# Kernel tuning notes

Measured on AMD Instinct MI355X. Metric: run time of the kernel, lower is better.

## Reference

```python
import jax, jax.numpy as jnp
import numpy as np

N_WIRES = 10
N_BLOCKS = 4
BATCH = 8192
FEAT = 4 * N_WIRES
DIM = 2 ** N_WIRES
BN_EPS = 1e-5

# sign of PauliZ on wire i for each basis state index (wire 0 = most significant bit,
# matching torchquantum's [bsz, 2, 2, ..., 2] state layout)
_k = np.arange(DIM)
_bits = (_k[None, :] >> (N_WIRES - 1 - np.arange(N_WIRES))[:, None]) & 1
SIGNS = jnp.asarray(1.0 - 2.0 * _bits, dtype=jnp.float32)  # [n_wires, 2^n]

H_GATE = jnp.array([[1, 1], [1, -1]], dtype=jnp.complex64) * jnp.complex64(0.70710678)
SX_GATE = jnp.complex64(0.5) * jnp.array([[1 + 1j, 1 - 1j], [1 - 1j, 1 + 1j]], dtype=jnp.complex64)


def rx_mat(theta):
    t = jnp.asarray(theta) * 0.5
    c = jnp.cos(t).astype(jnp.complex64)
    s = (-1j) * jnp.sin(t).astype(jnp.complex64)
    return jnp.stack([jnp.stack([c, s], -1), jnp.stack([s, c], -1)], -2)


def ry_mat(theta):
    t = jnp.asarray(theta) * 0.5
    c = jnp.cos(t).astype(jnp.complex64)
    s = jnp.sin(t).astype(jnp.complex64)
    return jnp.stack([jnp.stack([c, -s], -1), jnp.stack([s, c], -1)], -2)


def rz_mat(theta):
    e = jnp.exp(jnp.complex64(-0.5j) * jnp.asarray(theta).astype(jnp.complex64))
    z = jnp.zeros_like(e)
    return jnp.stack([jnp.stack([e, z], -1), jnp.stack([z, jnp.conj(e)], -1)], -2)


def apply_1q(state, gate, wire):
    # state: [B, 2, 2, ..., 2]; gate: [2,2] (shared) or [B,2,2] (per-sample encoder)
    s = jnp.moveaxis(state, wire + 1, -1)
    if gate.ndim == 3:
        s = jnp.einsum('bij,b...j->b...i', gate, s)
    else:
        s = jnp.einsum('ij,b...j->b...i', gate, s)
    return jnp.moveaxis(s, -1, wire + 1)


def apply_cnot(state, c, t):
    s = jnp.moveaxis(state, (c + 1, t + 1), (-2, -1))  # [..., ctrl, tgt]
    s = jnp.stack([s[..., 0, :], s[..., 1, ::-1]], axis=-2)
    return jnp.moveaxis(s, (-2, -1), (c + 1, t + 1))


def measure_all_z(state):
    probs = (state.real ** 2 + state.imag ** 2).reshape(state.shape[0], -1)  # [B, 2^n]
    return probs @ SIGNS.T  # [B, n_wires]


def encode(state, feats):
    # GeneralEncoder: per wire i apply rx, ry, rz, rx with data angles feats[:, 4i..4i+3]
    for i in range(N_WIRES):
        state = apply_1q(state, rx_mat(feats[:, 4 * i]), i)
        state = apply_1q(state, ry_mat(feats[:, 4 * i + 1]), i)
        state = apply_1q(state, rz_mat(feats[:, 4 * i + 2]), i)
        state = apply_1q(state, rx_mat(feats[:, 4 * i + 3]), i)
    return state


def qnn(feats, rz1, ry1, rz2, rz3):
    B = feats.shape[0]
    state = jnp.zeros((B, DIM), jnp.complex64).at[:, 0].set(1.0)
    state = state.reshape((B,) + (2,) * N_WIRES)
    for k in range(N_BLOCKS):
        for i in range(N_WIRES):
            state = apply_1q(state, rz_mat(rz1[k, i]), i)
        for i in range(N_WIRES):
            state = apply_1q(state, ry_mat(ry1[k, i]), i)
        for i in range(N_WIRES):
            state = apply_1q(state, rz_mat(rz2[k, i]), i)
        for i in range(N_WIRES):  # circular CNOT ring
            state = apply_cnot(state, i, (i + 1) % N_WIRES)
        if k != N_BLOCKS - 1:
            state = encode(state, feats)
    outs = [measure_all_z(state)]
    for i in range(N_WIRES):
        state = apply_1q(state, H_GATE, i)
    outs.append(measure_all_z(state))
    for i in range(N_WIRES):
        state = apply_1q(state, H_GATE, i)
        state = apply_1q(state, SX_GATE, i)
    outs.append(measure_all_z(state))
    for i in range(N_WIRES):  # only the last rz3 layer is applied in the source
        state = apply_1q(state, rz_mat(rz3[-1, i]), i)
    outs.append(measure_all_z(state))
    return jnp.concatenate(outs, axis=-1)  # [B, 4*n_wires]


def setup_inputs() -> dict:
    key = jax.random.key(0)
    ks = jax.random.split(key, 13)
    pi = np.float32(np.pi)
    w_scale = 1.0 / np.sqrt(np.float32(FEAT))
    return {
        'x': jax.random.normal(ks[0], (BATCH, FEAT), jnp.float32),
        'qlin_w': jax.random.normal(ks[1], (FEAT, FEAT), jnp.float32) * w_scale,
        'qlin_b': jax.random.normal(ks[2], (FEAT,), jnp.float32) * w_scale,
        'bn_gamma': jnp.ones((FEAT,), jnp.float32),
        'bn_beta': jnp.zeros((FEAT,), jnp.float32),
        'clin_w': jax.random.normal(ks[3], (FEAT, FEAT), jnp.float32) * w_scale,
        'clin_b': jax.random.normal(ks[4], (FEAT,), jnp.float32) * w_scale,
        'lin_w': jax.random.normal(ks[5], (FEAT, 2 * FEAT), jnp.float32) * w_scale,
        'lin_b': jax.random.normal(ks[6], (FEAT,), jnp.float32) * w_scale,
        'rz1': jax.random.uniform(ks[7], (N_BLOCKS, N_WIRES), jnp.float32, -pi, pi),
        'ry1': jax.random.uniform(ks[8], (N_BLOCKS, N_WIRES), jnp.float32, -pi, pi),
        'rz2': jax.random.uniform(ks[9], (N_BLOCKS, N_WIRES), jnp.float32, -pi, pi),
        'rz3': jax.random.uniform(ks[10], (N_BLOCKS, N_WIRES), jnp.float32, -pi, pi),
    }


def reference(x, qlin_w, qlin_b, bn_gamma, bn_beta, clin_w, clin_b, lin_w, lin_b, rz1, ry1, rz2, rz3):
    # quantum branch: Linear -> BatchNorm1d (training-mode batch stats) -> QNN
    xq = x @ qlin_w.T + qlin_b
    mu = xq.mean(axis=0)
    var = ((xq - mu) ** 2).mean(axis=0)  # biased variance, as torch BN
    xq = (xq - mu) * jax.lax.rsqrt(var + BN_EPS) * bn_gamma + bn_beta
    x1 = qnn(xq, rz1, ry1, rz2, rz3)
    # classical branch
    x2 = jax.nn.relu(x @ clin_w.T + clin_b)
    return jnp.concatenate([x1, x2], axis=-1) @ lin_w.T + lin_b
```

## Files before the change

### kernel.cpp

```cpp
#include <hip/hip_runtime.h>
#include <math.h>


typedef float v2f __attribute__((ext_vector_type(2)));
typedef unsigned uiv2 __attribute__((ext_vector_type(2)));

#define WS_XQ    0
#define WS_X1    327680
#define WS_PS1   327680
#define WS_PS2   368640
#define WS_BNA   655360
#define WS_BNC   655400
#define WS_GATES 655440

__device__ __forceinline__ float bperm1(int addr, float v){
  return __int_as_float(__builtin_amdgcn_ds_bpermute(addr, __float_as_int(v)));
}
__device__ __forceinline__ v2f bperm2(int addr, v2f v){
  v2f r; r.x = bperm1(addr, v.x); r.y = bperm1(addr, v.y); return r;
}
__device__ __forceinline__ v2f vs(float x){ return (v2f){x,x}; }

template<int C>
__device__ __forceinline__ float dppf(float x){
  return __int_as_float(__builtin_amdgcn_update_dpp(0, __float_as_int(x),
                                                    C, 0xf, 0xf, true));
}
#define QP_X1 0xB1
#define QP_X2 0x4E

__device__ __forceinline__ float xor1f(float x, int ){ return dppf<QP_X1>(x); }
__device__ __forceinline__ float xor2f(float x, int ){ return dppf<QP_X2>(x); }

template<int N>
__device__ __forceinline__ float xorshf(float x, int lane){
  float a = dppf<0x110+N>(x);
  float b = dppf<0x100+N>(x);
  return (lane & N) ? a : b;
}
__device__ __forceinline__ float xor4f(float x, int lane){ return xorshf<4>(x,lane); }
__device__ __forceinline__ float xor8f(float x, int lane){ return xorshf<8>(x,lane); }

#if __has_builtin(__builtin_amdgcn_permlane16_swap) && __has_builtin(__builtin_amdgcn_permlane32_swap)
__device__ __forceinline__ float xor16f(float x, int lane){
  uiv2 r = __builtin_amdgcn_permlane16_swap(__float_as_uint(x), __float_as_uint(x),
                                            false, false);
  return __uint_as_float((lane & 16) ? r.x : r.y);
}
__device__ __forceinline__ float xor32f(float x, int lane){
  uiv2 r = __builtin_amdgcn_permlane32_swap(__float_as_uint(x), __float_as_uint(x),
                                            false, false);
  return __uint_as_float((lane & 32) ? r.x : r.y);
}
#else
__device__ __forceinline__ float xor16f(float x, int lane){ return bperm1((lane^16)<<2, x); }
__device__ __forceinline__ float xor32f(float x, int lane){ return bperm1((lane^32)<<2, x); }
#endif

#define DEF_XORV(NAME, F1) \
__device__ __forceinline__ v2f NAME(v2f v, int lane){ \
  v2f r; r.x = F1(v.x,lane); r.y = F1(v.y,lane); return r; }
DEF_XORV(xor1v,  xor1f)
DEF_XORV(xor2v,  xor2f)
DEF_XORV(xor4v,  xor4f)
DEF_XORV(xor8v,  xor8f)
DEF_XORV(xor16v, xor16f)
DEF_XORV(xor32v, xor32f)

__device__ __forceinline__ float dsum(float x){
  x += dppf<0x111>(x);
  x += dppf<0x112>(x);
  x += dppf<0x114>(x);
  x += dppf<0x118>(x);
  x += dppf<0x142>(x);
  x += dppf<0x143>(x);
  return x;
}


#define DEF_GCROSS(NAME, PFN) \
__device__ __forceinline__ void NAME(v2f (&R)[8], v2f (&I)[8], int lane, bool hi, \
                                     const float* g){ \
  const float gar = hi ? g[6] : g[0], gai = hi ? g[7] : g[1]; \
  const float gbr = hi ? g[4] : g[2], gbi = hi ? g[5] : g[3]; \
  const v2f A=vs(gar), B=vs(gai), C=vs(gbr), D=vs(gbi); \
  _Pragma("unroll") \
  for (int p=0;p<8;++p){ \
    v2f PR = PFN(R[p],lane); \
    v2f PI = PFN(I[p],lane); \
    v2f nr = A*R[p] - B*I[p] + C*PR - D*PI; \
    v2f ni = A*I[p] + B*R[p] + C*PI + D*PR; \
    R[p]=nr; I[p]=ni; } \
}
DEF_GCROSS(g_cross_x32, xor32v)
DEF_GCROSS(g_cross_x16, xor16v)
DEF_GCROSS(g_cross_x8,  xor8v)
DEF_GCROSS(g_cross_x4,  xor4v)
DEF_GCROSS(g_cross_x2,  xor2v)
DEF_GCROSS(g_cross_x1,  xor1v)

template<int PM>
__device__ __forceinline__ void g_localp(v2f (&R)[8], v2f (&I)[8], const float* g)
{
  const v2f g00r=vs(g[0]), g00i=vs(g[1]), g01r=vs(g[2]), g01i=vs(g[3]);
  const v2f g10r=vs(g[4]), g10i=vs(g[5]), g11r=vs(g[6]), g11i=vs(g[7]);
#pragma unroll
  for (int p=0;p<8;++p) if (!(p&PM)) {
    const int q = p|PM;
    v2f r0=R[p], i0=I[p], r1=R[q], i1=I[q];
    R[p] = g00r*r0 - g00i*i0 + g01r*r1 - g01i*i1;
    I[p] = g00r*i0 + g00i*r0 + g01r*i1 + g01i*r1;
    R[q] = g10r*r0 - g10i*i0 + g11r*r1 - g11i*i1;
    I[q] = g10r*i0 + g10i*r0 + g11r*i1 + g11i*r1;
  }
}

__device__ __forceinline__ void g_local9(v2f (&R)[8], v2f (&I)[8], const float* g)
{
  const v2f Gr0 = (v2f){g[0], g[4]};
  const v2f Gi0 = (v2f){g[1], g[5]};
  const v2f Gr1 = (v2f){g[2], g[6]};
  const v2f Gi1 = (v2f){g[3], g[7]};
#pragma unroll
  for (int p=0;p<8;++p) {
    v2f Rx = vs(R[p].x), Ix = vs(I[p].x);
    v2f Ry = vs(R[p].y), Iy = vs(I[p].y);
    R[p] = Gr0*Rx - Gi0*Ix + Gr1*Ry - Gi1*Iy;
    I[p] = Gr0*Ix + Gi0*Rx + Gr1*Iy + Gi1*Ry;
  }
}

__device__ __forceinline__ void cnot_ring(v2f (&R)[8], v2f (&I)[8],
                                          int addrg, int lane, bool c5)
{
#pragma unroll
  for (int p=0;p<8;++p) R[p] = bperm2(addrg, R[p]);
#pragma unroll
  for (int p=0;p<8;++p) I[p] = bperm2(addrg, I[p]);
#pragma unroll
  for (int p=0;p<4;++p) {
    v2f a=R[p], b=R[p|4];
    R[p]   = c5 ? b : a;
    R[p|4] = c5 ? a : b;
    v2f ai=I[p], bi=I[p|4];
    I[p]   = c5 ? bi : ai;
    I[p|4] = c5 ? ai : bi;
  }
#pragma unroll
  for (int p=0;p<8;++p) if ((p&4)&&!(p&2)) {
    const int q=p|2;
    v2f t=R[p]; R[p]=R[q]; R[q]=t;
    t=I[p]; I[p]=I[q]; I[q]=t;
  }
#pragma unroll
  for (int p=0;p<8;++p) if ((p&2)&&!(p&1)) {
    const int q=p|1;
    v2f t=R[p]; R[p]=R[q]; R[q]=t;
    t=I[p]; I[p]=I[q]; I[q]=t;
  }
#pragma unroll
  for (int p=1;p<8;p+=2) {
    R[p] = __builtin_shufflevector(R[p],R[p],1,0);
    I[p] = __builtin_shufflevector(I[p],I[p],1,0);
  }
#pragma unroll
  for (int p=0;p<8;++p) {
    R[p].y = xor32f(R[p].y, lane);
    I[p].y = xor32f(I[p].y, lane);
  }
}


__global__ __launch_bounds__(320) void k_xq(const float* __restrict__ x,
                     const float* __restrict__ w, const float* __restrict__ b,
                     float* __restrict__ xq, float* __restrict__ ps1, float* __restrict__ ps2)
{
  __shared__ float wlds[40*41];
  __shared__ float xlds[320];
  __shared__ float accs[320];
  const int t = threadIdx.x;
  const int sl = t/40, f = t - sl*40;
  const int s0 = blockIdx.x*8;
#pragma unroll
  for (int i=0;i<5;++i) {
    int idx = t + i*320;
    int ff = idx/40, kk = idx - ff*40;
    wlds[ff*41+kk] = w[idx];
  }
  xlds[t] = x[s0*40 + t];
  __syncthreads();
  float acc = b[f];
#pragma unroll
  for (int k=0;k<40;++k) acc = fmaf(xlds[sl*40+k], wlds[f*41+k], acc);
  xq[s0*40 + t] = acc;
  accs[t] = acc;
  __syncthreads();
  if (t < 40) {
    float s1=0.f, s2=0.f;
#pragma unroll
    for (int m=0;m<8;++m){ float vv=accs[m*40+t]; s1+=vv; s2=fmaf(vv,vv,s2); }
    ps1[t*1024 + blockIdx.x] = s1;
    ps2[t*1024 + blockIdx.x] = s2;
  }
}

__global__ void k_bn(const float* __restrict__ ps1, const float* __restrict__ ps2,
                     const float* __restrict__ gamma, const float* __restrict__ beta,
                     const float* __restrict__ rz1, const float* __restrict__ ry1,
                     const float* __restrict__ rz2,
                     float* __restrict__ bn_a, float* __restrict__ bn_c,
                     float* __restrict__ gates)
{
  const int f = blockIdx.x, t = threadIdx.x;
  if (f == 40) {
    if (t < 40) {
      float g = rz1[t], a = ry1[t], b = rz2[t];
      float ca, sa, cp, sp, cm, sm;
      sincosf(0.5f*a, &sa, &ca);
      sincosf(0.5f*(b+g), &sp, &cp);
      sincosf(0.5f*(b-g), &sm, &cm);
      float* G = gates + t*8;
      G[0]= ca*cp; G[1]=-ca*sp;
      G[2]=-sa*cm; G[3]= sa*sm;
      G[4]= sa*cm; G[5]= sa*sm;
      G[6]= ca*cp; G[7]= ca*sp;
    }
    return;
  }
  float s1=0.f, s2=0.f;
#pragma unroll
  for (int i=0;i<4;++i){ s1 += ps1[f*1024 + t + i*256]; s2 += ps2[f*1024 + t + i*256]; }
  __shared__ float a1[256], a2[256];
  a1[t]=s1; a2[t]=s2; __syncthreads();
  for (int off=128; off; off>>=1){
    if (t<off){ a1[t]+=a1[t+off]; a2[t]+=a2[t+off]; }
    __syncthreads();
  }
  if (t==0) {
    float mu = a1[0]*(1.f/8192.f);
    float var = a2[0]*(1.f/8192.f) - mu*mu;
    float a = gamma[f]*rsqrtf(var + 1e-5f);
    bn_a[f]=a; bn_c[f]=beta[f]-mu*a;
  }
}

#define GEN10(PTR) \
  g_cross_x32(R,I,lane,h0,(PTR)+0);  g_cross_x16(R,I,lane,h1,(PTR)+8);  \
  g_cross_x8 (R,I,lane,h2,(PTR)+16); g_cross_x4 (R,I,lane,h3,(PTR)+24); \
  g_cross_x2 (R,I,lane,h4,(PTR)+32); g_cross_x1 (R,I,lane,h5,(PTR)+40); \
  g_localp<4>(R,I,(PTR)+48);   g_localp<2>(R,I,(PTR)+56);   \
  g_localp<1>(R,I,(PTR)+64);   g_local9(R,I,(PTR)+72);

__global__ __launch_bounds__(256) void k_qnn(const float* __restrict__ xq,
    const float* __restrict__ bn_a, const float* __restrict__ bn_c,
    const float* __restrict__ gates, float* __restrict__ x1)
{
  const int tix  = threadIdx.x;
  const int lane = tix & 63;
  const int wv   = tix >> 6;
  const int s    = blockIdx.x*4 + wv;

  __shared__ float Ebuf[4][10][8];
  __shared__ float Fbuf[4][3][10][8];

  if (lane < 10) {
    const int i = lane;
    const int f = 4*i;
    float h0 = 0.5f * fmaf(xq[s*40+f+0], bn_a[f+0], bn_c[f+0]);
    float h1 = 0.5f * fmaf(xq[s*40+f+1], bn_a[f+1], bn_c[f+1]);
    float h2 = 0.5f * fmaf(xq[s*40+f+2], bn_a[f+2], bn_c[f+2]);
    float h3 = 0.5f * fmaf(xq[s*40+f+3], bn_a[f+3], bn_c[f+3]);
    float c0,s0,c1,s1,c2,s2,c3,s3;
    sincosf(h0,&s0,&c0); sincosf(h1,&s1,&c1);
    sincosf(h2,&s2,&c2); sincosf(h3,&s3,&c3);
    float A00r=c1*c0, A00i= s1*s0;
    float A01r=-s1*c0, A01i=-c1*s0;
    float A10r= s1*c0, A10i=-c1*s0;
    float A11r= c1*c0, A11i=-s1*s0;
    float B00r = A00r*c2 + A00i*s2, B00i = A00i*c2 - A00r*s2;
    float B01r = A01r*c2 + A01i*s2, B01i = A01i*c2 - A01r*s2;
    float B10r = A10r*c2 - A10i*s2, B10i = A10i*c2 + A10r*s2;
    float B11r = A11r*c2 - A11i*s2, B11i = A11i*c2 + A11r*s2;
    float* e = &Ebuf[wv][i][0];
    e[0] = c3*B00r + s3*B10i;  e[1] = c3*B00i - s3*B10r;
    e[2] = c3*B01r + s3*B11i;  e[3] = c3*B01i - s3*B11r;
    e[4] = c3*B10r + s3*B00i;  e[5] = c3*B10i - s3*B00r;
    e[6] = c3*B11r + s3*B01i;  e[7] = c3*B11i - s3*B01r;
  }

  if (lane < 30) {
    const int k = lane/10, i = lane - k*10;
    const float* U = gates + (k+1)*80 + i*8;
    const float* E = &Ebuf[wv][i][0];
    float u00r=U[0],u00i=U[1],u01r=U[2],u01i=U[3],u10r=U[4],u10i=U[5],u11r=U[6],u11i=U[7];
    float e00r=E[0],e00i=E[1],e01r=E[2],e01i=E[3],e10r=E[4],e10i=E[5],e11r=E[6],e11i=E[7];
    float* F = &Fbuf[wv][k][i][0];
    F[0] = u00r*e00r - u00i*e00i + u01r*e10r - u01i*e10i;
    F[1] = u00r*e00i + u00i*e00r + u01r*e10i + u01i*e10r;
    F[2] = u00r*e01r - u00i*e01i + u01r*e11r - u01i*e11i;
    F[3] = u00r*e01i + u00i*e01r + u01r*e11i + u01i*e11r;
    F[4] = u10r*e00r - u10i*e00i + u11r*e10r - u11i*e10i;
    F[5] = u10r*e00i + u10i*e00r + u11r*e10i + u11i*e10r;
    F[6] = u10r*e01r - u10i*e01i + u11r*e11r - u11i*e11i;
    F[7] = u10r*e01i + u10i*e01r + u11r*e11i + u11i*e11r;
  }

  const bool h0 = (lane & 32) != 0;
  const bool h1 = (lane & 16) != 0;
  const bool h2 = (lane &  8) != 0;
  const bool h3 = (lane &  4) != 0;
  const bool h4 = (lane &  2) != 0;
  const bool h5 = (lane &  1) != 0;
  const int addrg = (lane ^ (lane >> 1)) << 2;

  v2f R[8], I[8];
  {
    float cr = 1.f, ci = 0.f;
#pragma unroll
    for (int w=0; w<6; ++w) {
      const float g0r = gates[w*8+0], g0i = gates[w*8+1];
      const float g1r = gates[w*8+4], g1i = gates[w*8+5];
      const bool bset = (lane >> (5-w)) & 1;
      const float ar = bset ? g1r : g0r, ai = bset ? g1i : g0i;
      const float tr = cr*ar - ci*ai, ti = cr*ai + ci*ar;
      cr = tr; ci = ti;
    }
    float p67r[4], p67i[4], p89r[4], p89i[4];
#pragma unroll
    for (int b6=0;b6<2;++b6)
#pragma unroll
      for (int b7=0;b7<2;++b7) {
        const float x6r = gates[6*8 + 4*b6], x6i = gates[6*8 + 4*b6 + 1];
        const float x7r = gates[7*8 + 4*b7], x7i = gates[7*8 + 4*b7 + 1];
        p67r[b6*2+b7] = x6r*x7r - x6i*x7i;
        p67i[b6*2+b7] = x6r*x7i + x6i*x7r;
      }
#pragma unroll
    for (int b8=0;b8<2;++b8)
#pragma unroll
      for (int b9=0;b9<2;++b9) {
        const float x8r = gates[8*8 + 4*b8], x8i = gates[8*8 + 4*b8 + 1];
        const float x9r = gates[9*8 + 4*b9], x9i = gates[9*8 + 4*b9 + 1];
        p89r[b8*2+b9] = x8r*x9r - x8i*x9i;
        p89i[b8*2+b9] = x8r*x9i + x8i*x9r;
      }
#pragma unroll
    for (int m=0;m<4;++m) {
      const float tr = p67r[m]*cr - p67i[m]*ci;
      const float ti = p67r[m]*ci + p67i[m]*cr;
      p67r[m]=tr; p67i[m]=ti;
    }
#pragma unroll
    for (int p=0;p<8;++p) {
      const int hi = p>>1, b8 = p&1;
      const v2f Pr = (v2f){p89r[2*b8], p89r[2*b8+1]};
      const v2f Pi = (v2f){p89i[2*b8], p89i[2*b8+1]};
      R[p] = vs(p67r[hi])*Pr - vs(p67i[hi])*Pi;
      I[p] = vs(p67r[hi])*Pi + vs(p67i[hi])*Pr;
    }
  }

  cnot_ring(R,I,addrg,lane,h5);
  { const float* F = &Fbuf[wv][0][0][0]; GEN10(F) }
  cnot_ring(R,I,addrg,lane,h5);
  { const float* F = &Fbuf[wv][1][0][0]; GEN10(F) }
  cnot_ring(R,I,addrg,lane,h5);
  { const float* F = &Fbuf[wv][2][0][0]; GEN10(F) }
  cnot_ring(R,I,addrg,lane,h5);

  float* dst = x1 + s*40;

  {
    v2f pv[8];
#pragma unroll
    for (int p=0;p<8;++p) pv[p] = R[p]*R[p] + I[p]*I[p];
    v2f T8 = (pv[0]-pv[1]) + (pv[2]-pv[3]) + (pv[4]-pv[5]) + (pv[6]-pv[7]);
    v2f aa[4];
#pragma unroll
    for (int m=0;m<4;++m) aa[m] = pv[2*m] + pv[2*m+1];
    v2f T7 = (aa[0]-aa[1]) + (aa[2]-aa[3]);
    v2f T6 = (aa[0]+aa[1]) - (aa[2]+aa[3]);
    v2f S  = (aa[0]+aa[1]) + (aa[2]+aa[3]);
    float q8 = T8.x + T8.y;
    float q7 = T7.x + T7.y;
    float q6 = T6.x + T6.y;
    float q9 = S.x - S.y;
    float P  = S.x + S.y;

    float v = P;
    { float pt = xor1f (v,lane); v = h5 ? (pt - v) : (pt + v); }
    { float pt = xor2f (v,lane); v = h4 ? (pt - v) : (pt + v); }
    { float pt = xor4f (v,lane); v = h3 ? (pt - v) : (pt + v); }
    { float pt = xor8f (v,lane); v = h2 ? (pt - v) : (pt + v); }
    { float pt = xor16f(v,lane); v = h1 ? (pt - v) : (pt + v); }
    { float pt = xor32f(v,lane); v = h0 ? (pt - v) : (pt + v); }

    q6 = dsum(q6); q7 = dsum(q7); q8 = dsum(q8); q9 = dsum(q9);

    if (lane==32) dst[0]=v;
    if (lane==16) dst[1]=v;
    if (lane== 8) dst[2]=v;
    if (lane== 4) dst[3]=v;
    if (lane== 2) dst[4]=v;
    if (lane== 1) dst[5]=v;
    if (lane==63){ dst[6]=q6; dst[7]=q7; dst[8]=q8; dst[9]=q9; }
  }

#define XYC(PFN,HW,W) { \
    v2f U=vs(0.f), V=vs(0.f); \
    _Pragma("unroll") \
    for (int p=0;p<8;++p) { \
      v2f PR = PFN(R[p],lane); \
      v2f PI = PFN(I[p],lane); \
      U += R[p]*PR + I[p]*PI; \
      V += I[p]*PR - R[p]*PI; \
    } \
    float u = U.x + U.y; \
    float vv = V.x + V.y; \
    vv = (HW) ? vv : -vv; \
    u = dsum(u); vv = dsum(vv); \
    if (lane==63){ dst[10+(W)]=u; dst[20+(W)]=vv; dst[30+(W)]=vv; } \
  }
  XYC(xor32v,h0,0) XYC(xor16v,h1,1) XYC(xor8v,h2,2)
  XYC(xor4v ,h3,3) XYC(xor2v ,h4,4) XYC(xor1v,h5,5)
#undef XYC

#define XYL(PM,W) { \
    v2f U=vs(0.f), V=vs(0.f); \
    _Pragma("unroll") \
    for (int p=0;p<8;++p) if (!(p&(PM))) { \
      const int q=p|(PM); \
      U += R[p]*R[q] + I[p]*I[q]; \
      V += I[p]*R[q] - R[p]*I[q]; \
    } \
    float u = U.x + U.y; \
    float vv = V.x + V.y; \
    u = dsum(u); vv = dsum(vv); \
    if (lane==63){ dst[10+(W)]=2.f*u; float y=-2.f*vv; dst[20+(W)]=y; dst[30+(W)]=y; } \
  }
  XYL(4,6) XYL(2,7) XYL(1,8)
#undef XYL

  {
    float u=0.f, vv=0.f;
#pragma unroll
    for (int p=0;p<8;++p) {
      u  = fmaf(R[p].x, R[p].y, u);  u  = fmaf(I[p].x, I[p].y, u);
      vv = fmaf(I[p].x, R[p].y, vv); vv = fmaf(-R[p].x, I[p].y, vv);
    }
    u = dsum(u); vv = dsum(vv);
    if (lane==63){ dst[19]=2.f*u; float y=-2.f*vv; dst[29]=y; dst[39]=y; }
  }
}

__global__ void k_epi(const float* __restrict__ x, const float* __restrict__ x1,
                      const float* __restrict__ clin_w, const float* __restrict__ clin_b,
                      const float* __restrict__ lin_w, const float* __restrict__ lin_b,
                      float* __restrict__ out)
{
  const int t = threadIdx.x;
  const int sl = t/40, f = t - sl*40;
  const int s = blockIdx.x*8 + sl;
  __shared__ float x2s[8][40];
  float acc = clin_b[f];
#pragma unroll
  for (int k=0;k<40;++k) acc = fmaf(x[s*40+k], clin_w[f*40+k], acc);
  x2s[sl][f] = fmaxf(acc, 0.f);
  __syncthreads();
  float o = lin_b[f];
#pragma unroll
  for (int j=0;j<40;++j) o = fmaf(x1[s*40+j], lin_w[f*80+j], o);
#pragma unroll
  for (int j=0;j<40;++j) o = fmaf(x2s[sl][j], lin_w[f*80+40+j], o);
  out[s*40+f] = o;
}

extern "C" void kernel_launch(void* const* d_in, const int* in_sizes, int n_in,
                              void* d_out, int out_size, void* d_ws, size_t ws_size,
                              hipStream_t stream)
{
  const float* x      = (const float*)d_in[0];
  const float* qlin_w = (const float*)d_in[1];
  const float* qlin_b = (const float*)d_in[2];
  const float* bn_g   = (const float*)d_in[3];
  const float* bn_b   = (const float*)d_in[4];
  const float* clin_w = (const float*)d_in[5];
  const float* clin_b = (const float*)d_in[6];
  const float* lin_w  = (const float*)d_in[7];
  const float* lin_b  = (const float*)d_in[8];
  const float* rz1    = (const float*)d_in[9];
  const float* ry1    = (const float*)d_in[10];
  const float* rz2    = (const float*)d_in[11];

  float* ws    = (float*)d_ws;
  float* xq    = ws + WS_XQ;
  float* x1    = ws + WS_X1;
  float* ps1   = ws + WS_PS1;
  float* ps2   = ws + WS_PS2;
  float* bn_a  = ws + WS_BNA;
  float* bn_c  = ws + WS_BNC;
  float* gates = ws + WS_GATES;
  float* out   = (float*)d_out;

  hipLaunchKernelGGL(k_xq,  dim3(1024), dim3(320), 0, stream, x, qlin_w, qlin_b, xq, ps1, ps2);
  hipLaunchKernelGGL(k_bn,  dim3(41),   dim3(256), 0, stream, ps1, ps2, bn_g, bn_b,
                     rz1, ry1, rz2, bn_a, bn_c, gates);
  hipLaunchKernelGGL(k_qnn, dim3(2048), dim3(256), 0, stream, xq, bn_a, bn_c, gates, x1);
  hipLaunchKernelGGL(k_epi, dim3(1024), dim3(320), 0, stream, x, x1, clin_w, clin_b, lin_w, lin_b, out);
}
```

Baseline: 177.5 us.

## Fuse linear, gate setup and epilogue into QNN kernel; compute BN stats directly

Replaces the four-kernel pipeline with two kernels. A 40-block stats kernel recomputes each quantum-linear feature over the whole batch to get the BN mean and variance. The QNN kernel then recomputes the quantum linear per sample, builds the rotation gates in shared memory, and fuses the classical branch and final linear layer, so the xq and x1 workspace round trips and two launches go away. The cost is extra recomputation: the stats kernel reads x 40 times on only 40 blocks, and every QNN block repeats the gate sincos.

Measured after the change: 197.5 us. +11.3%, slower.

```diff
diff --git a/kernel.cpp b/kernel.cpp
--- a/kernel.cpp
+++ b/kernel.cpp
@@ -4,14 +4,6 @@
 
 typedef float v2f __attribute__((ext_vector_type(2)));
 typedef unsigned uiv2 __attribute__((ext_vector_type(2)));
-
-#define WS_XQ    0
-#define WS_X1    327680
-#define WS_PS1   327680
-#define WS_PS2   368640
-#define WS_BNA   655360
-#define WS_BNC   655400
-#define WS_GATES 655440
 
 __device__ __forceinline__ float bperm1(int addr, float v){
   return __int_as_float(__builtin_amdgcn_ds_bpermute(addr, __float_as_int(v)));
@@ -170,79 +162,46 @@
   }
 }
 
-
-__global__ __launch_bounds__(320) void k_xq(const float* __restrict__ x,
-                     const float* __restrict__ w, const float* __restrict__ b,
-                     float* __restrict__ xq, float* __restrict__ ps1, float* __restrict__ ps2)
-{
-  __shared__ float wlds[40*41];
-  __shared__ float xlds[320];
-  __shared__ float accs[320];
-  const int t = threadIdx.x;
-  const int sl = t/40, f = t - sl*40;
-  const int s0 = blockIdx.x*8;
-#pragma unroll
-  for (int i=0;i<5;++i) {
-    int idx = t + i*320;
-    int ff = idx/40, kk = idx - ff*40;
-    wlds[ff*41+kk] = w[idx];
-  }
-  xlds[t] = x[s0*40 + t];
-  __syncthreads();
-  float acc = b[f];
-#pragma unroll
-  for (int k=0;k<40;++k) acc = fmaf(xlds[sl*40+k], wlds[f*41+k], acc);
-  xq[s0*40 + t] = acc;
-  accs[t] = acc;
-  __syncthreads();
-  if (t < 40) {
-    float s1=0.f, s2=0.f;
-#pragma unroll
-    for (int m=0;m<8;++m){ float vv=accs[m*40+t]; s1+=vv; s2=fmaf(vv,vv,s2); }
-    ps1[t*1024 + blockIdx.x] = s1;
-    ps2[t*1024 + blockIdx.x] = s2;
-  }
-}
-
-__global__ void k_bn(const float* __restrict__ ps1, const float* __restrict__ ps2,
-                     const float* __restrict__ gamma, const float* __restrict__ beta,
-                     const float* __restrict__ rz1, const float* __restrict__ ry1,
-                     const float* __restrict__ rz2,
-                     float* __restrict__ bn_a, float* __restrict__ bn_c,
-                     float* __restrict__ gates)
+__global__ __launch_bounds__(1024) void k_pre(const float* __restrict__ x,
+    const float* __restrict__ qw, const float* __restrict__ qb,
+    const float* __restrict__ gamma, const float* __restrict__ beta,
+    float* __restrict__ bn_a, float* __restrict__ bn_c)
 {
   const int f = blockIdx.x, t = threadIdx.x;
-  if (f == 40) {
-    if (t < 40) {
-      float g = rz1[t], a = ry1[t], b = rz2[t];
-      float ca, sa, cp, sp, cm, sm;
-      sincosf(0.5f*a, &sa, &ca);
-      sincosf(0.5f*(b+g), &sp, &cp);
-      sincosf(0.5f*(b-g), &sm, &cm);
-      float* G = gates + t*8;
-      G[0]= ca*cp; G[1]=-ca*sp;
-      G[2]=-sa*cm; G[3]= sa*sm;
-      G[4]= sa*cm; G[5]= sa*sm;
-      G[6]= ca*cp; G[7]= ca*sp;
-    }
-    return;
-  }
-  float s1=0.f, s2=0.f;
-#pragma unroll
-  for (int i=0;i<4;++i){ s1 += ps1[f*1024 + t + i*256]; s2 += ps2[f*1024 + t + i*256]; }
-  __shared__ float a1[256], a2[256];
-  a1[t]=s1; a2[t]=s2; __syncthreads();
-  for (int off=128; off; off>>=1){
-    if (t<off){ a1[t]+=a1[t+off]; a2[t]+=a2[t+off]; }
-    __syncthreads();
-  }
-  if (t==0) {
-    float mu = a1[0]*(1.f/8192.f);
-    float var = a2[0]*(1.f/8192.f) - mu*mu;
-    float a = gamma[f]*rsqrtf(var + 1e-5f);
-    bn_a[f]=a; bn_c[f]=beta[f]-mu*a;
-  }
-}
+  __shared__ float wf[40];
+  __shared__ float a1[16], a2[16];
+  if (t < 40) wf[t] = qw[f*40 + t];
+  __syncthreads();
+  const float bf = qb[f];
+  float s1 = 0.f, s2 = 0.f;
+  for (int s = t; s < 8192; s += 1024) {
+    const float4* xr = (const float4*)(x + s*40);
+    float d = bf;
+#pragma unroll
+    for (int q = 0; q < 10; ++q) {
+      float4 v = xr[q];
+      d = fmaf(v.x, wf[4*q+0], d);
+      d = fmaf(v.y, wf[4*q+1], d);
+      d = fmaf(v.z, wf[4*q+2], d);
+      d = fmaf(v.w, wf[4*q+3], d);
+    }
+    s1 += d; s2 = fmaf(d, d, s2);
+  }
+  s1 = dsum(s1); s2 = dsum(s2);
+  const int lane = t & 63, wid = t >> 6;
+  if (lane == 63) { a1[wid] = s1; a2[wid] = s2; }
+  __syncthreads();
+  if (t == 0) {
+    float t1 = 0.f, t2 = 0.f;
+#pragma unroll
+    for (int i = 0; i < 16; ++i) { t1 += a1[i]; t2 += a2[i]; }
+    float mu  = t1 * (1.f/8192.f);
+    float var = t2 * (1.f/8192.f) - mu*mu;
+    float a = gamma[f] * rsqrtf(var + 1e-5f);
+    bn_a[f] = a; bn_c[f] = beta[f] - mu*a;
+  }
+}
+
 
 #define GEN10(PTR) \
   g_cross_x32(R,I,lane,h0,(PTR)+0);  g_cross_x16(R,I,lane,h1,(PTR)+8);  \
@@ -251,25 +210,69 @@
   g_localp<4>(R,I,(PTR)+48);   g_localp<2>(R,I,(PTR)+56);   \
   g_localp<1>(R,I,(PTR)+64);   g_local9(R,I,(PTR)+72);
 
-__global__ __launch_bounds__(256) void k_qnn(const float* __restrict__ xq,
+__global__ __launch_bounds__(256) void k_qnn(const float* __restrict__ x,
+    const float* __restrict__ qlin_w, const float* __restrict__ qlin_b,
     const float* __restrict__ bn_a, const float* __restrict__ bn_c,
-    const float* __restrict__ gates, float* __restrict__ x1)
+    const float* __restrict__ rz1, const float* __restrict__ ry1,
+    const float* __restrict__ rz2,
+    const float* __restrict__ clin_w, const float* __restrict__ clin_b,
+    const float* __restrict__ lin_w, const float* __restrict__ lin_b,
+    float* __restrict__ out)
 {
   const int tix  = threadIdx.x;
   const int lane = tix & 63;
   const int wv   = tix >> 6;
   const int s    = blockIdx.x*4 + wv;
 
+  __shared__ float Gbuf[40][8];
   __shared__ float Ebuf[4][10][8];
   __shared__ float Fbuf[4][3][10][8];
+  __shared__ float xs [4][40];
+  __shared__ float xqs[4][40];
+  __shared__ float x1s[4][40];
+  __shared__ float x2s[4][40];
+
+  if (tix < 160) xs[tix/40][tix%40] = x[blockIdx.x*160 + tix];
+  {
+    const int gi = tix - 160;
+    if (gi >= 0 && gi < 40) {
+      float g = rz1[gi], ay = ry1[gi], bz = rz2[gi];
+      float ca, sa, cp, sp, cm, sm;
+      sincosf(0.5f*ay, &sa, &ca);
+      sincosf(0.5f*(bz+g), &sp, &cp);
+      sincosf(0.5f*(bz-g), &sm, &cm);
+      float* G = &Gbuf[gi][0];
+      G[0]= ca*cp; G[1]=-ca*sp;
+      G[2]=-sa*cm; G[3]= sa*sm;
+      G[4]= sa*cm; G[5]= sa*sm;
+      G[6]= ca*cp; G[7]= ca*sp;
+    }
+  }
+  __syncthreads();
+
+  if (tix < 160) {
+    const int sl = tix/40, f = tix - sl*40;
+    const float4* qw = (const float4*)(qlin_w + f*40);
+    float acc = qlin_b[f];
+#pragma unroll
+    for (int q = 0; q < 10; ++q) {
+      float4 v = qw[q];
+      acc = fmaf(v.x, xs[sl][4*q+0], acc);
+      acc = fmaf(v.y, xs[sl][4*q+1], acc);
+      acc = fmaf(v.z, xs[sl][4*q+2], acc);
+      acc = fmaf(v.w, xs[sl][4*q+3], acc);
+    }
+    xqs[sl][f] = acc;
+  }
+  __syncthreads();
 
   if (lane < 10) {
     const int i = lane;
     const int f = 4*i;
-    float h0 = 0.5f * fmaf(xq[s*40+f+0], bn_a[f+0], bn_c[f+0]);
-    float h1 = 0.5f * fmaf(xq[s*40+f+1], bn_a[f+1], bn_c[f+1]);
-    float h2 = 0.5f * fmaf(xq[s*40+f+2], bn_a[f+2], bn_c[f+2]);
-    float h3 = 0.5f * fmaf(xq[s*40+f+3], bn_a[f+3], bn_c[f+3]);
+    float h0 = 0.5f * fmaf(xqs[wv][f+0], bn_a[f+0], bn_c[f+0]);
+    float h1 = 0.5f * fmaf(xqs[wv][f+1], bn_a[f+1], bn_c[f+1]);
+    float h2 = 0.5f * fmaf(xqs[wv][f+2], bn_a[f+2], bn_c[f+2]);
+    float h3 = 0.5f * fmaf(xqs[wv][f+3], bn_a[f+3], bn_c[f+3]);
     float c0,s0,c1,s1,c2,s2,c3,s3;
     sincosf(h0,&s0,&c0); sincosf(h1,&s1,&c1);
     sincosf(h2,&s2,&c2); sincosf(h3,&s3,&c3);
@@ -290,7 +293,7 @@
 
   if (lane < 30) {
     const int k = lane/10, i = lane - k*10;
-    const float* U = gates + (k+1)*80 + i*8;
+    const float* U = &Gbuf[(k+1)*10 + i][0];
     const float* E = &Ebuf[wv][i][0];
     float u00r=U[0],u00i=U[1],u01r=U[2],u01i=U[3],u10r=U[4],u10i=U[5],u11r=U[6],u11i=U[7];
     float e00r=E[0],e00i=E[1],e01r=E[2],e01i=E[3],e10r=E[4],e10i=E[5],e11r=E[6],e11i=E[7];
@@ -318,8 +321,8 @@
     float cr = 1.f, ci = 0.f;
 #pragma unroll
     for (int w=0; w<6; ++w) {
-      const float g0r = gates[w*8+0], g0i = gates[w*8+1];
-      const float g1r = gates[w*8+4], g1i = gates[w*8+5];
+      const float g0r = Gbuf[w][0], g0i = Gbuf[w][1];
+      const float g1r = Gbuf[w][4], g1i = Gbuf[w][5];
       const bool bset = (lane >> (5-w)) & 1;
       const float ar = bset ? g1r : g0r, ai = bset ? g1i : g0i;
       const float tr = cr*ar - ci*ai, ti = cr*ai + ci*ar;
@@ -330,8 +333,8 @@
     for (int b6=0;b6<2;++b6)
 #pragma unroll
       for (int b7=0;b7<2;++b7) {
-        const float x6r = gates[6*8 + 4*b6], x6i = gates[6*8 + 4*b6 + 1];
-        const float x7r = gates[7*8 + 4*b7], x7i = gates[7*8 + 4*b7 + 1];
+        const float x6r = Gbuf[6][4*b6], x6i = Gbuf[6][4*b6+1];
+        const float x7r = Gbuf[7][4*b7], x7i = Gbuf[7][4*b7+1];
         p67r[b6*2+b7] = x6r*x7r - x6i*x7i;
         p67i[b6*2+b7] = x6r*x7i + x6i*x7r;
       }
@@ -339,8 +342,8 @@
     for (int b8=0;b8<2;++b8)
 #pragma unroll
       for (int b9=0;b9<2;++b9) {
-        const float x8r = gates[8*8 + 4*b8], x8i = gates[8*8 + 4*b8 + 1];
-        const float x9r = gates[9*8 + 4*b9], x9i = gates[9*8 + 4*b9 + 1];
+        const float x8r = Gbuf[8][4*b8], x8i = Gbuf[8][4*b8+1];
+        const float x9r = Gbuf[9][4*b9], x9i = Gbuf[9][4*b9+1];
         p89r[b8*2+b9] = x8r*x9r - x8i*x9i;
         p89i[b8*2+b9] = x8r*x9i + x8i*x9r;
       }
@@ -368,7 +371,7 @@
   { const float* F = &Fbuf[wv][2][0][0]; GEN10(F) }
   cnot_ring(R,I,addrg,lane,h5);
 
-  float* dst = x1 + s*40;
+  float* dst = &x1s[wv][0];
 
   {
     v2f pv[8];
@@ -451,28 +454,45 @@
     u = dsum(u); vv = dsum(vv);
     if (lane==63){ dst[19]=2.f*u; float y=-2.f*vv; dst[29]=y; dst[39]=y; }
   }
-}
-
-__global__ void k_epi(const float* __restrict__ x, const float* __restrict__ x1,
-                      const float* __restrict__ clin_w, const float* __restrict__ clin_b,
-                      const float* __restrict__ lin_w, const float* __restrict__ lin_b,
-                      float* __restrict__ out)
-{
-  const int t = threadIdx.x;
-  const int sl = t/40, f = t - sl*40;
-  const int s = blockIdx.x*8 + sl;
-  __shared__ float x2s[8][40];
-  float acc = clin_b[f];
-#pragma unroll
-  for (int k=0;k<40;++k) acc = fmaf(x[s*40+k], clin_w[f*40+k], acc);
-  x2s[sl][f] = fmaxf(acc, 0.f);
+
   __syncthreads();
-  float o = lin_b[f];
-#pragma unroll
-  for (int j=0;j<40;++j) o = fmaf(x1[s*40+j], lin_w[f*80+j], o);
-#pragma unroll
-  for (int j=0;j<40;++j) o = fmaf(x2s[sl][j], lin_w[f*80+40+j], o);
-  out[s*40+f] = o;
+  if (tix < 160) {
+    const int sl = tix/40, f = tix - sl*40;
+    const float4* cw = (const float4*)(clin_w + f*40);
+    float acc = clin_b[f];
+#pragma unroll
+    for (int q = 0; q < 10; ++q) {
+      float4 v = cw[q];
+      acc = fmaf(v.x, xs[sl][4*q+0], acc);
+      acc = fmaf(v.y, xs[sl][4*q+1], acc);
+      acc = fmaf(v.z, xs[sl][4*q+2], acc);
+      acc = fmaf(v.w, xs[sl][4*q+3], acc);
+    }
+    x2s[sl][f] = fmaxf(acc, 0.f);
+  }
+  __syncthreads();
+  if (tix < 160) {
+    const int sl = tix/40, f = tix - sl*40;
+    const float4* lw = (const float4*)(lin_w + f*80);
+    float o = lin_b[f];
+#pragma unroll
+    for (int q = 0; q < 10; ++q) {
+      float4 v = lw[q];
+      o = fmaf(v.x, x1s[sl][4*q+0], o);
+      o = fmaf(v.y, x1s[sl][4*q+1], o);
+      o = fmaf(v.z, x1s[sl][4*q+2], o);
+      o = fmaf(v.w, x1s[sl][4*q+3], o);
+    }
+#pragma unroll
+    for (int q = 10; q < 20; ++q) {
+      float4 v = lw[q];
+      o = fmaf(v.x, x2s[sl][4*(q-10)+0], o);
+      o = fmaf(v.y, x2s[sl][4*(q-10)+1], o);
+      o = fmaf(v.z, x2s[sl][4*(q-10)+2], o);
+      o = fmaf(v.w, x2s[sl][4*(q-10)+3], o);
+    }
+    out[blockIdx.x*160 + tix] = o;
+  }
 }
 
 extern "C" void kernel_launch(void* const* d_in, const int* in_sizes, int n_in,
@@ -492,19 +512,14 @@
   const float* ry1    = (const float*)d_in[10];
   const float* rz2    = (const float*)d_in[11];
 
-  float* ws    = (float*)d_ws;
-  float* xq    = ws + WS_XQ;
-  float* x1    = ws + WS_X1;
-  float* ps1   = ws + WS_PS1;
-  float* ps2   = ws + WS_PS2;
-  float* bn_a  = ws + WS_BNA;
-  float* bn_c  = ws + WS_BNC;
-  float* gates = ws + WS_GATES;
-  float* out   = (float*)d_out;
-
-  hipLaunchKernelGGL(k_xq,  dim3(1024), dim3(320), 0, stream, x, qlin_w, qlin_b, xq, ps1, ps2);
-  hipLaunchKernelGGL(k_bn,  dim3(41),   dim3(256), 0, stream, ps1, ps2, bn_g, bn_b,
-                     rz1, ry1, rz2, bn_a, bn_c, gates);
-  hipLaunchKernelGGL(k_qnn, dim3(2048), dim3(256), 0, stream, xq, bn_a, bn_c, gates, x1);
-  hipLaunchKernelGGL(k_epi, dim3(1024), dim3(320), 0, stream, x, x1, clin_w, clin_b, lin_w, lin_b, out);
-}
+  float* ws   = (float*)d_ws;
+  float* bn_a = ws;
+  float* bn_c = ws + 40;
+  float* out  = (float*)d_out;
+
+  hipLaunchKernelGGL(k_pre, dim3(40),   dim3(1024), 0, stream,
+                     x, qlin_w, qlin_b, bn_g, bn_b, bn_a, bn_c);
+  hipLaunchKernelGGL(k_qnn, dim3(2048), dim3(256),  0, stream,
+                     x, qlin_w, qlin_b, bn_a, bn_c, rz1, ry1, rz2,
+                     clin_w, clin_b, lin_w, lin_b, out);
+}
```
